# Kernel optimization log

Hardware: AMD Instinct MI355X
Metric: run time of the kernel (lower is better)

The kernel has to match this reference:

```python
import jax, jax.numpy as jnp
import numpy as np

GRID_SIZE, SPLINE_ORDER = 5, 3  # efficient-kan KANLinear defaults
NUM_BASES = GRID_SIZE + SPLINE_ORDER


def b_splines(x, grid):
    # x: (N, in_dim), grid: (in_dim, GRID_SIZE + 2*SPLINE_ORDER + 1)
    xe = x[..., None]
    bases = ((xe >= grid[:, :-1]) & (xe < grid[:, 1:])).astype(x.dtype)
    for k in range(1, SPLINE_ORDER + 1):  # Cox-de Boor recursion (static, 3 iters)
        left = (xe - grid[:, : -(k + 1)]) / (grid[:, k:-1] - grid[:, : -(k + 1)])
        right = (grid[:, k + 1:] - xe) / (grid[:, k + 1:] - grid[:, 1:-k])
        bases = left * bases[..., :-1] + right * bases[..., 1:]
    return bases  # (N, in_dim, NUM_BASES)


def kan_linear(x, grid, base_w, spline_w, scaler):
    # base branch: SiLU(x) @ W_base^T ; spline branch: B-spline basis @ scaled spline weights
    n = x.shape[0]
    out_dim = base_w.shape[0]
    base = jax.nn.silu(x) @ base_w.T
    bs = b_splines(x, grid).reshape(n, -1)                    # (N, in*NUM_BASES)
    sw = (spline_w * scaler[..., None]).reshape(out_dim, -1)  # (out, in*NUM_BASES)
    return base + bs @ sw.T


def setup_inputs() -> dict:
    key = jax.random.key(0)
    N, E, F, H, C, L = 50000, 500000, 128, 128, 40, 3
    ks = jax.random.split(key, 8)
    x = jax.random.normal(ks[0], (N, F), dtype=jnp.float32)
    edge_index = jax.random.randint(ks[1], (2, E), 0, N)
    # KAN grid (registered buffer in efficient-kan): uniform over [-1,1] extended by spline_order
    h_step = 2.0 / GRID_SIZE
    pts = np.arange(-SPLINE_ORDER, GRID_SIZE + SPLINE_ORDER + 1) * h_step - 1.0
    grid_mp = jnp.asarray(np.tile(pts, (F, 1)), dtype=jnp.float32)
    D = F + L * H  # skip-concat dim into output KANLinear
    grid_out = jnp.asarray(np.tile(pts, (D, 1)), dtype=jnp.float32)
    s = 0.1
    conv_base_w = jax.random.normal(ks[2], (L, H, F), dtype=jnp.float32) * s
    conv_spline_w = jax.random.normal(ks[3], (L, H, F, NUM_BASES), dtype=jnp.float32) * s
    conv_scaler = jnp.ones((L, H, F), dtype=jnp.float32)
    conv_bias = jnp.zeros((L, H), dtype=jnp.float32)
    bn_gamma = jnp.ones((L, H), dtype=jnp.float32)
    bn_beta = jnp.zeros((L, H), dtype=jnp.float32)
    out_base_w = jax.random.normal(ks[4], (C, D), dtype=jnp.float32) * s
    out_spline_w = jax.random.normal(ks[5], (C, D, NUM_BASES), dtype=jnp.float32) * s
    out_scaler = jnp.ones((C, D), dtype=jnp.float32)
    return dict(x=x, edge_index=edge_index, grid_mp=grid_mp, conv_base_w=conv_base_w,
                conv_spline_w=conv_spline_w, conv_scaler=conv_scaler, conv_bias=conv_bias,
                bn_gamma=bn_gamma, bn_beta=bn_beta, grid_out=grid_out,
                out_base_w=out_base_w, out_spline_w=out_spline_w, out_scaler=out_scaler)


def reference(x, edge_index, grid_mp, conv_base_w, conv_spline_w, conv_scaler, conv_bias,
              bn_gamma, bn_beta, grid_out, out_base_w, out_spline_w, out_scaler):
    N = x.shape[0]
    L = conv_base_w.shape[0]
    # GCN normalization with self-loops (computed once; identical each layer)
    loop = jnp.arange(N)
    src = jnp.concatenate([edge_index[0], loop])
    dst = jnp.concatenate([edge_index[1], loop])
    deg = jax.ops.segment_sum(jnp.ones_like(src, dtype=x.dtype), dst, num_segments=N)
    dinv = jnp.where(deg > 0, jax.lax.rsqrt(jnp.maximum(deg, 1.0)), 0.0)
    norm = dinv[src] * dinv[dst]  # (E+N,)
    feats = [x]
    for i in range(L):  # static layer loop
        h = kan_linear(x, grid_mp, conv_base_w[i], conv_spline_w[i], conv_scaler[i])
        # symmetric-normalized sparse aggregation (gather on src, scatter-add on dst)
        h = jax.ops.segment_sum(h[src] * norm[:, None], dst, num_segments=N) + conv_bias[i]
        # BatchNorm1d (training mode: biased batch statistics over nodes)
        mu = h.mean(axis=0)
        var = h.var(axis=0)
        x = (h - mu) * jax.lax.rsqrt(var + 1e-5) * bn_gamma[i] + bn_beta[i]
        feats.append(x)  # dropout p=0.0 is identity
    xc = jnp.concatenate(feats, axis=1)  # skip-concat: (N, F + L*H)
    logits = kan_linear(xc, grid_out, out_base_w, out_spline_w, out_scaler)
    return jax.nn.log_softmax(logits, axis=1)
```

## Files before the change

### kernel.cpp

```cpp
#include <hip/hip_runtime.h>
#include <hip/hip_bf16.h>
#include <math.h>

#define F_IN   128
#define HID    128
#define NLAYER 3
#define NCLS   40
#define DCAT   512
#define OOUT   64

typedef short s16x8 __attribute__((ext_vector_type(8)));
typedef unsigned short u16x8 __attribute__((ext_vector_type(8)));
typedef unsigned short u16x4 __attribute__((ext_vector_type(4)));
typedef float f32x4 __attribute__((ext_vector_type(4)));
typedef unsigned long long u64x2 __attribute__((ext_vector_type(2)));


static __device__ __forceinline__ float silu_f(float x) {
    return x / (1.f + __expf(-x));
}

static __device__ __forceinline__ unsigned short f2bf_rn(float f) {
    union { __hip_bfloat16 h; unsigned short u; } cv;
    cv.h = __float2bfloat16(f);
    return cv.u;
}

static __device__ __forceinline__ void lds_barrier() {
    asm volatile("s_waitcnt lgkmcnt(0)" ::: "memory");
    __builtin_amdgcn_s_barrier();
}


__global__ __launch_bounds__(256) void deg_init_kernel(int* deg, int N) {
    for (int i = blockIdx.x * blockDim.x + threadIdx.x; i < N; i += gridDim.x * blockDim.x)
        deg[i] = 1;
}

__global__ __launch_bounds__(256) void deg_count_kernel(const int* __restrict__ dst, int E, int* deg) {
    for (int i = blockIdx.x * blockDim.x + threadIdx.x; i < E; i += gridDim.x * blockDim.x)
        atomicAdd(&deg[dst[i]], 1);
}

__global__ __launch_bounds__(256) void dinv_kernel(const int* __restrict__ deg, float* dinv, int N) {
    for (int i = blockIdx.x * blockDim.x + threadIdx.x; i < N; i += gridDim.x * blockDim.x)
        dinv[i] = rsqrtf((float)deg[i]);
}

__global__ __launch_bounds__(256) void scan_reduce_kernel(const int* __restrict__ deg, int* __restrict__ bsum, int N) {
    __shared__ int sh[256];
    int t = threadIdx.x;
    int e = blockIdx.x * 256 + t;
    sh[t] = (e < N) ? deg[e] : 0;
    __syncthreads();
#pragma unroll
    for (int off = 128; off > 0; off >>= 1) {
        if (t < off) sh[t] += sh[t + off];
        __syncthreads();
    }
    if (t == 0) bsum[blockIdx.x] = sh[0];
}

__global__ __launch_bounds__(256) void scan_top_kernel(const int* __restrict__ bsum, int* __restrict__ bbase, int nsb) {
    __shared__ int sh[256];
    int t = threadIdx.x;
    int chunk = (nsb + 255) >> 8;
    int begin = t * chunk;
    int end = begin + chunk; if (end > nsb) end = nsb;
    int s = 0;
    for (int i = begin; i < end; ++i) s += bsum[i];
    sh[t] = s;
    __syncthreads();
#pragma unroll
    for (int off = 1; off < 256; off <<= 1) {
        int v = 0;
        if (t >= off) v = sh[t - off];
        __syncthreads();
        if (t >= off) sh[t] += v;
        __syncthreads();
    }
    int run = (t == 0) ? 0 : sh[t - 1];
    for (int i = begin; i < end; ++i) {
        bbase[i] = run;
        run += bsum[i];
    }
}

__global__ __launch_bounds__(256) void scan_write_kernel(const int* __restrict__ deg,
                                                         const int* __restrict__ bbase,
                                                         int* __restrict__ offs, int* __restrict__ cursor, int N) {
    __shared__ int sh[256];
    int t = threadIdx.x;
    int e = blockIdx.x * 256 + t;
    int d = (e < N) ? deg[e] : 0;
    sh[t] = d;
    __syncthreads();
#pragma unroll
    for (int off = 1; off < 256; off <<= 1) {
        int v = 0;
        if (t >= off) v = sh[t - off];
        __syncthreads();
        if (t >= off) sh[t] += v;
        __syncthreads();
    }
    int incl = sh[t] + bbase[blockIdx.x];
    int excl = incl - d;
    if (e < N) {
        offs[e] = excl;
        cursor[e] = excl;
        if (e == N - 1) offs[N] = incl;
    }
}

__global__ __launch_bounds__(256) void fill_kernel(const int* __restrict__ src, const int* __restrict__ dst,
                                                   int E, int N, int* cursor, int* __restrict__ csr) {
    int total = E + N;
    for (int i = blockIdx.x * blockDim.x + threadIdx.x; i < total; i += gridDim.x * blockDim.x) {
        if (i < E) {
            int d = dst[i];
            int p = atomicAdd(&cursor[d], 1);
            csr[p] = src[i];
        } else {
            int n = i - E;
            int p = atomicAdd(&cursor[n], 1);
            csr[p] = n;
        }
    }
}

__global__ __launch_bounds__(256) void pack_conv_mfma(const float* __restrict__ bw,
                                                      const float* __restrict__ sw,
                                                      const float* __restrict__ sc,
                                                      unsigned short* __restrict__ wpk) {
    int total = NLAYER * 9 * 4 * 8 * 64 * 8;
    for (int idx = blockIdx.x * blockDim.x + threadIdx.x; idx < total; idx += gridDim.x * blockDim.x) {
        int e    = idx & 7;
        int lane = (idx >> 3) & 63;
        int cf   = (idx >> 9) & 7;
        int kk   = (idx >> 12) & 3;
        int cc   = (idx >> 14) % 9;
        int l    = idx / (9 << 14);
        int o = cf * 16 + (lane & 15);
        int k = kk * 32 + ((lane >> 4) << 3) + e;
        float v;
        if (cc == 8) {
            v = bw[(l * 128 + o) * 128 + k];
        } else {
            int f = cc * 16 + (k >> 3);
            int j = k & 7;
            int base = (l * 128 + o) * 128 + f;
            v = sw[base * 8 + j] * sc[base];
        }
        wpk[idx] = f2bf_rn(v);
    }
}

__global__ __launch_bounds__(256) void pack_out_mfma(const float* __restrict__ bw,
                                                     const float* __restrict__ sw,
                                                     const float* __restrict__ sc,
                                                     unsigned short* __restrict__ wpk) {
    int total = 36 * 4 * 4 * 64 * 8;
    for (int idx = blockIdx.x * blockDim.x + threadIdx.x; idx < total; idx += gridDim.x * blockDim.x) {
        int e    = idx & 7;
        int lane = (idx >> 3) & 63;
        int cf   = (idx >> 9) & 3;
        int kk   = (idx >> 11) & 3;
        int gcc  = idx >> 13;
        int g = gcc / 9, cc = gcc % 9;
        int o = cf * 16 + (lane & 15);
        int k = kk * 32 + ((lane >> 4) << 3) + e;
        float v = 0.f;
        if (o < NCLS) {
            if (cc == 8) {
                int f = g * 128 + k;
                v = bw[o * DCAT + f];
            } else {
                int f = g * 128 + cc * 16 + (k >> 3);
                int j = k & 7;
                int base = o * DCAT + f;
                v = sw[base * 8 + j] * sc[base];
            }
        }
        wpk[idx] = f2bf_rn(v);
    }
}


__global__ __launch_bounds__(512) void affine_init_kernel(float* scA, float* shA) {
    int i = threadIdx.x;
    scA[i] = 1.f; shA[i] = 0.f;
}

template<bool CONV, bool INIT>
__global__ __launch_bounds__(256, 2) void kan_fused_kernel(
    const float* __restrict__ xin, int xstride, int in_off,
    const float* __restrict__ scA, const float* __restrict__ shA,
    const unsigned short* __restrict__ wconv,
    const unsigned short* __restrict__ wout,
    unsigned short* __restrict__ htmp,
    const float* __restrict__ dinv,
    float* __restrict__ out_acc, int N) {

    __shared__ __align__(16) char lds_phi0[16384];
    __shared__ __align__(16) char lds_phi1[16384];

    const int tid = threadIdx.x;
    const int lane = tid & 63;
    const int wave = tid >> 6;
    const int l15 = lane & 15, lg = lane >> 4;
    const int nblk = blockIdx.x * 64;

    const float g0 = -1.f - 3.f * 0.4f;
    const float invh = 1.f / 0.4f;

    const int fg = tid & 3;
    const int n0 = tid >> 2;

    f32x4 accc[4][2];
    f32x4 acco[4];
    if (CONV) {
#pragma unroll
        for (int r = 0; r < 4; ++r)
#pragma unroll
            for (int c = 0; c < 2; ++c) accc[r][c] = (f32x4)0.f;
    }
#pragma unroll
    for (int r = 0; r < 4; ++r) acco[r] = (f32x4)0.f;

    float4 xqb[2], scb[2], shb[2];
    auto ldx = [&](int cc, int slot) {
        int f0 = in_off + cc * 16 + fg * 4;
        scb[slot] = *(const float4*)(scA + f0);
        shb[slot] = *(const float4*)(shA + f0);
        int gn = nblk + n0;
        xqb[slot] = (gn < N) ? *(const float4*)(xin + (size_t)gn * xstride + f0)
                             : (float4){0.f, 0.f, 0.f, 0.f};
    };

    s16x8 wc_reg[4][2];
    s16x8 wo_reg[4];
    auto loadW = [&](int cc) {
        if (CONV) {
            const unsigned short* wcb = wconv + (size_t)cc * 16384;
#pragma unroll
            for (int kk = 0; kk < 4; ++kk)
#pragma unroll
                for (int c = 0; c < 2; ++c) {
                    int cf = wave * 2 + c;
                    wc_reg[kk][c] = *(const s16x8*)(wcb + (((size_t)kk * 8 + cf) * 64 + lane) * 8);
                }
        }
        const unsigned short* wob = wout + (size_t)cc * 8192;
#pragma unroll
        for (int kk = 0; kk < 4; ++kk)
            wo_reg[kk] = *(const s16x8*)(wob + (((size_t)kk * 4 + wave) * 64 + lane) * 8);
    };

    u16x4 sreg[8];

    u64x2 pcur[4];
    auto phi_compute = [&](int ccc, int slot) {
        float xi[4] = {xqb[slot].x, xqb[slot].y, xqb[slot].z, xqb[slot].w};
        float scr[4] = {scb[slot].x, scb[slot].y, scb[slot].z, scb[slot].w};
        float shr[4] = {shb[slot].x, shb[slot].y, shb[slot].z, shb[slot].w};
        u16x4 sv;
#pragma unroll
        for (int fl = 0; fl < 4; ++fl) {
            float y = fmaf(xi[fl], scr[fl], shr[fl]);
            sv[fl] = f2bf_rn(silu_f(y));
            float t = (y - g0) * invh;
            float cfl = floorf(t);
            int c = (int)cfl;
            c = c < -20 ? -20 : (c > 20 ? 20 : c);
            float u = t - cfl;
            float um = 1.f - u;
            float u2 = u * u;
            float um2 = um * um;
            float w0 = um2 * um * (1.f / 6.f);
            float w3 = u2 * u * (1.f / 6.f);
            float w1 = fmaf(fmaf(0.5f, u, -1.f), u2, 2.f / 3.f);
            float w2 = fmaf(fmaf(-0.5f, u, 0.5f), u2, fmaf(0.5f, u, 1.f / 6.f));
            unsigned long long W = (unsigned long long)f2bf_rn(w0)
                                 | ((unsigned long long)f2bf_rn(w1) << 16)
                                 | ((unsigned long long)f2bf_rn(w2) << 32)
                                 | ((unsigned long long)f2bf_rn(w3) << 48);
            int pos = (c - 3) * 16;
            unsigned long long lo = (pos >= 0) ? (W << (pos & 63)) : (W >> ((-pos) & 63));
            lo = (pos >= 64 || pos <= -64) ? 0ull : lo;
            int ph = pos - 64;
            unsigned long long hi = (ph >= 0) ? (W << (ph & 63)) : (W >> ((-ph) & 63));
            hi = (ph >= 64 || ph <= -64) ? 0ull : hi;
            u64x2 v; v.x = lo; v.y = hi;
            pcur[fl] = v;
        }
        sreg[ccc] = sv;
    };

    auto write_phi = [&](char* buf) {
        int swz = (n0 & 7) << 4;
#pragma unroll
        for (int i = 0; i < 4; ++i) {
            int byte = n0 * 256 + ((fg * 64 + i * 16) ^ swz);
            *(u64x2*)(buf + byte) = pcur[i];
        }
    };

    auto write_silu = [&](char* buf) {
        int swz = (n0 & 7) << 4;
#pragma unroll
        for (int ccc = 0; ccc < 8; ++ccc) {
            int byte = n0 * 256 + (((ccc * 16 + fg * 4) * 2) ^ swz);
            *(u16x4*)(buf + byte) = sreg[ccc];
        }
    };

    auto mfma_phase = [&](const char* buf) {
#pragma unroll
        for (int kk = 0; kk < 4; ++kk) {
            const int kb = kk * 64 + lg * 16;
            s16x8 af[4];
#pragma unroll
            for (int r = 0; r < 4; ++r) {
                int n = r * 16 + l15;
                af[r] = *(const s16x8*)(buf + n * 256 + (kb ^ ((n & 7) << 4)));
            }
            if (CONV) {
#pragma unroll
                for (int c = 0; c < 2; ++c)
#pragma unroll
                    for (int r = 0; r < 4; ++r)
                        accc[r][c] = __builtin_amdgcn_mfma_f32_16x16x32_bf16(af[r], wc_reg[kk][c], accc[r][c], 0, 0, 0);
            }
#pragma unroll
            for (int r = 0; r < 4; ++r)
                acco[r] = __builtin_amdgcn_mfma_f32_16x16x32_bf16(af[r], wo_reg[kk], acco[r], 0, 0, 0);
        }
    };

    ldx(0, 0);
    phi_compute(0, 0);
    ldx(1, 1);
    loadW(0);
    write_phi(lds_phi0);
    __syncthreads();

#pragma unroll
    for (int cc = 0; cc < 9; ++cc) {
        char* cur = (cc & 1) ? lds_phi1 : lds_phi0;
        char* nxt = (cc & 1) ? lds_phi0 : lds_phi1;
        if (cc < 7) ldx(cc + 2, cc & 1);
        mfma_phase(cur);
        if (cc < 8) loadW(cc + 1);
        if (cc < 7) {
            phi_compute(cc + 1, (cc + 1) & 1);
            write_phi(nxt);
        }
        if (cc == 7) write_silu(nxt);
        if (cc < 8) lds_barrier();
    }

#pragma unroll
    for (int r = 0; r < 4; ++r) {
        int nb = nblk + r * 16 + lg * 4;
        if (CONV) {
#pragma unroll
            for (int c = 0; c < 2; ++c) {
                int o = wave * 32 + c * 16 + l15;
#pragma unroll
                for (int q = 0; q < 4; ++q) {
                    int n = nb + q;
                    if (n < N) htmp[(size_t)n * HID + o] = f2bf_rn(accc[r][c][q] * dinv[n]);
                }
            }
        }
        {
            int o = wave * 16 + l15;
            if (o < NCLS) {
#pragma unroll
                for (int q = 0; q < 4; ++q) {
                    int n = nb + q;
                    if (n < N) {
                        size_t a = (size_t)n * OOUT + o;
                        float v = acco[r][q];
                        if (!INIT) v += out_acc[a];
                        out_acc[a] = v;
                    }
                }
            }
        }
    }
}

__global__ __launch_bounds__(256) void agg_kernel(const unsigned short* __restrict__ h,
                                                  const float* __restrict__ dinv,
                                                  const int* __restrict__ offs,
                                                  const int* __restrict__ csr,
                                                  const float* __restrict__ bias,
                                                  float* __restrict__ xc, int out_off, int N) {
    int n = blockIdx.x * 4 + (threadIdx.x >> 6);
    if (n >= N) return;
    int lane = threadIdx.x & 63;
    int s = offs[n], e = offs[n + 1];
    float s0[8], s1[8];
#pragma unroll
    for (int k = 0; k < 8; ++k) { s0[k] = 0.f; s1[k] = 0.f; }
    int i = s;
    for (; i + 8 <= e; i += 8) {
        int vv[8];
#pragma unroll
        for (int k = 0; k < 8; ++k) vv[k] = csr[i + k];
        unsigned uu[8];
#pragma unroll
        for (int k = 0; k < 8; ++k) uu[k] = *(const unsigned*)(h + (size_t)vv[k] * HID + lane * 2);
#pragma unroll
        for (int k = 0; k < 8; ++k) {
            s0[k] += __uint_as_float(uu[k] << 16);
            s1[k] += __uint_as_float(uu[k] & 0xffff0000u);
        }
    }
    for (; i < e; ++i) {
        int v = csr[i];
        unsigned u = *(const unsigned*)(h + (size_t)v * HID + lane * 2);
        s0[0] += __uint_as_float(u << 16);
        s1[0] += __uint_as_float(u & 0xffff0000u);
    }
    float a0 = ((s0[0] + s0[1]) + (s0[2] + s0[3])) + ((s0[4] + s0[5]) + (s0[6] + s0[7]));
    float a1 = ((s1[0] + s1[1]) + (s1[2] + s1[3])) + ((s1[4] + s1[5]) + (s1[6] + s1[7]));
    float dn = dinv[n];
    float2 bv = *(const float2*)(bias + lane * 2);
    float2 res = {fmaf(a0, dn, bv.x), fmaf(a1, dn, bv.y)};
    *(float2*)(xc + (size_t)n * DCAT + out_off + lane * 2) = res;
}

__global__ __launch_bounds__(128) void bn_stats_kernel(const float* __restrict__ xc, int off, int N,
                                                       float* __restrict__ bnsum, float* __restrict__ bnsq) {
    int f = threadIdx.x;
    float s = 0.f, q = 0.f;
    for (int n = blockIdx.x; n < N; n += gridDim.x) {
        float v = xc[(size_t)n * DCAT + off + f];
        s += v;
        q += v * v;
    }
    atomicAdd(&bnsum[f], s);
    atomicAdd(&bnsq[f], q);
}

__global__ __launch_bounds__(128) void bn_affine_kernel(const float* __restrict__ bnsum,
                                                        const float* __restrict__ bnsq,
                                                        const float* __restrict__ gamma,
                                                        const float* __restrict__ beta,
                                                        float* scA, float* shA, int seg_off, float invN) {
    int f = threadIdx.x;
    float mu = bnsum[f] * invN;
    float var = bnsq[f] * invN - mu * mu;
    float rs = rsqrtf(var + 1e-5f);
    float s = gamma[f] * rs;
    scA[seg_off + f] = s;
    shA[seg_off + f] = fmaf(-mu, s, beta[f]);
}

__global__ __launch_bounds__(256) void logsoftmax_kernel(const float* __restrict__ oacc,
                                                         float* __restrict__ out, int N) {
    for (int n = blockIdx.x * blockDim.x + threadIdx.x; n < N; n += gridDim.x * blockDim.x) {
        const float* row = oacc + (size_t)n * OOUT;
        float m = -1e30f;
#pragma unroll
        for (int j = 0; j < NCLS; ++j) m = fmaxf(m, row[j]);
        float s = 0.f;
#pragma unroll
        for (int j = 0; j < NCLS; ++j) s += __expf(row[j] - m);
        float lse = m + __logf(s);
        float* orow = out + (size_t)n * NCLS;
#pragma unroll
        for (int j = 0; j < NCLS; ++j) orow[j] = row[j] - lse;
    }
}


extern "C" void kernel_launch(void* const* d_in, const int* in_sizes, int n_in,
                              void* d_out, int out_size, void* d_ws, size_t ws_size,
                              hipStream_t stream) {
    const float* x            = (const float*)d_in[0];
    const int*   eidx         = (const int*)d_in[1];
    const float* conv_base_w  = (const float*)d_in[3];
    const float* conv_spline_w= (const float*)d_in[4];
    const float* conv_scaler  = (const float*)d_in[5];
    const float* conv_bias    = (const float*)d_in[6];
    const float* bn_gamma     = (const float*)d_in[7];
    const float* bn_beta      = (const float*)d_in[8];
    const float* out_base_w   = (const float*)d_in[10];
    const float* out_spline_w = (const float*)d_in[11];
    const float* out_scaler   = (const float*)d_in[12];
    float* out = (float*)d_out;

    int N = in_sizes[0] / F_IN;
    int E = in_sizes[1] / 2;
    const int* esrc = eidx;
    const int* edst = eidx + E;

    int blocks = (N + 63) / 64;
    int npad = blocks * 64;
    int nsb = (N + 255) / 256;

    char* p = (char*)d_ws;
    auto carve = [&](size_t bytes) {
        char* r = p;
        p += (bytes + 255) & ~(size_t)255;
        return r;
    };
    float* xc   = (float*)carve((size_t)N * DCAT * 4);
    unsigned short* htmp = (unsigned short*)carve((size_t)npad * HID * 2);
    float* oacc = (float*)carve((size_t)npad * OOUT * 4);
    float* dinv = (float*)carve((size_t)N * 4);
    float* bn   = (float*)carve((size_t)NLAYER * 2 * HID * 4);
    float* scA  = (float*)carve((size_t)DCAT * 4);
    float* shA  = (float*)carve((size_t)DCAT * 4);
    unsigned short* wpkc = (unsigned short*)carve((size_t)NLAYER * 9 * 128 * 128 * 2);
    unsigned short* wpko = (unsigned short*)carve((size_t)36 * 64 * 128 * 2);
    int* deg    = (int*)carve((size_t)N * 4);
    int* offs   = (int*)carve((size_t)(N + 1) * 4);
    int* cursor = (int*)carve((size_t)(N + 1) * 4);
    int* bsum   = (int*)carve((size_t)nsb * 4);
    int* bbase  = (int*)carve((size_t)nsb * 4);
    int* csr    = (int*)carve((size_t)(E + N) * 4);

    hipMemsetAsync(bn, 0, NLAYER * 2 * HID * 4, stream);

    deg_init_kernel<<<512, 256, 0, stream>>>(deg, N);
    deg_count_kernel<<<1024, 256, 0, stream>>>(edst, E, deg);
    dinv_kernel<<<512, 256, 0, stream>>>(deg, dinv, N);
    scan_reduce_kernel<<<nsb, 256, 0, stream>>>(deg, bsum, N);
    scan_top_kernel<<<1, 256, 0, stream>>>(bsum, bbase, nsb);
    scan_write_kernel<<<nsb, 256, 0, stream>>>(deg, bbase, offs, cursor, N);
    fill_kernel<<<1024, 256, 0, stream>>>(esrc, edst, E, N, cursor, csr);

    pack_conv_mfma<<<1024, 256, 0, stream>>>(conv_base_w, conv_spline_w, conv_scaler, wpkc);
    pack_out_mfma<<<1024, 256, 0, stream>>>(out_base_w, out_spline_w, out_scaler, wpko);
    affine_init_kernel<<<1, 512, 0, stream>>>(scA, shA);

    float invN = 1.f / (float)N;
    for (int l = 0; l < NLAYER; ++l) {
        int in_off = l * HID;
        int out_off = (l + 1) * HID;
        const unsigned short* wl = wpkc + (size_t)l * 9 * 16384;
        const unsigned short* wo = wpko + (size_t)l * 9 * 8192;
        if (l == 0)
            kan_fused_kernel<true, true><<<blocks, 256, 0, stream>>>(
                x, F_IN, 0, scA, shA, wl, wo, htmp, dinv, oacc, N);
        else
            kan_fused_kernel<true, false><<<blocks, 256, 0, stream>>>(
                xc, DCAT, in_off, scA, shA, wl, wo, htmp, dinv, oacc, N);
        agg_kernel<<<(N + 3) / 4, 256, 0, stream>>>(htmp, dinv, offs, csr, conv_bias + l * HID, xc, out_off, N);
        float* bnsum = bn + l * 2 * HID;
        float* bnsq  = bnsum + HID;
        bn_stats_kernel<<<256, 128, 0, stream>>>(xc, out_off, N, bnsum, bnsq);
        bn_affine_kernel<<<1, 128, 0, stream>>>(bnsum, bnsq, bn_gamma + l * HID, bn_beta + l * HID,
                                                scA, shA, out_off, invN);
    }

    kan_fused_kernel<false, false><<<blocks, 256, 0, stream>>>(
        xc, DCAT, 384, scA, shA, nullptr, wpko + (size_t)3 * 9 * 8192, htmp, dinv, oacc, N);

    logsoftmax_kernel<<<(N + 255) / 256, 256, 0, stream>>>(oacc, out, N);
}
```

Measured before the change: 532.3 us.

## Split aggregation wavefront into four edge groups with 16-byte row loads

```diff
diff --git a/kernel.cpp b/kernel.cpp
--- a/kernel.cpp
+++ b/kernel.cpp
@@ -24,6 +24,10 @@
     union { __hip_bfloat16 h; unsigned short u; } cv;
     cv.h = __float2bfloat16(f);
     return cv.u;
+}
+
+static __device__ __forceinline__ float bf2f(unsigned short u) {
+    return __uint_as_float((unsigned)u << 16);
 }
 
 static __device__ __forceinline__ void lds_barrier() {
@@ -400,36 +404,64 @@
     int n = blockIdx.x * 4 + (threadIdx.x >> 6);
     if (n >= N) return;
     int lane = threadIdx.x & 63;
+    int eg = lane >> 4;
+    int cg = lane & 15;
     int s = offs[n], e = offs[n + 1];
-    float s0[8], s1[8];
-#pragma unroll
-    for (int k = 0; k < 8; ++k) { s0[k] = 0.f; s1[k] = 0.f; }
-    int i = s;
-    for (; i + 8 <= e; i += 8) {
-        int vv[8];
-#pragma unroll
-        for (int k = 0; k < 8; ++k) vv[k] = csr[i + k];
-        unsigned uu[8];
-#pragma unroll
-        for (int k = 0; k < 8; ++k) uu[k] = *(const unsigned*)(h + (size_t)vv[k] * HID + lane * 2);
-#pragma unroll
-        for (int k = 0; k < 8; ++k) {
-            s0[k] += __uint_as_float(uu[k] << 16);
-            s1[k] += __uint_as_float(uu[k] & 0xffff0000u);
-        }
-    }
-    for (; i < e; ++i) {
-        int v = csr[i];
-        unsigned u = *(const unsigned*)(h + (size_t)v * HID + lane * 2);
-        s0[0] += __uint_as_float(u << 16);
-        s1[0] += __uint_as_float(u & 0xffff0000u);
-    }
-    float a0 = ((s0[0] + s0[1]) + (s0[2] + s0[3])) + ((s0[4] + s0[5]) + (s0[6] + s0[7]));
-    float a1 = ((s1[0] + s1[1]) + (s1[2] + s1[3])) + ((s1[4] + s1[5]) + (s1[6] + s1[7]));
-    float dn = dinv[n];
-    float2 bv = *(const float2*)(bias + lane * 2);
-    float2 res = {fmaf(a0, dn, bv.x), fmaf(a1, dn, bv.y)};
-    *(float2*)(xc + (size_t)n * DCAT + out_off + lane * 2) = res;
+
+    float acc[4][8];
+#pragma unroll
+    for (int a = 0; a < 4; ++a)
+#pragma unroll
+        for (int k = 0; k < 8; ++k) acc[a][k] = 0.f;
+
+    for (int base = s; base < e; base += 64) {
+        int cnt = e - base; if (cnt > 64) cnt = 64;
+        int ci = base + lane;
+        int cv = (ci < e) ? csr[ci] : 0;
+
+#pragma unroll
+        for (int j = 0; j < 4; ++j) {
+            int ei = j * 4 + eg;
+            int v = __shfl(cv, ei);
+            if (ei < cnt) {
+                u16x8 hv = *(const u16x8*)(h + (size_t)v * HID + cg * 8);
+#pragma unroll
+                for (int k = 0; k < 8; ++k) acc[j][k] += bf2f(hv[k]);
+            }
+        }
+        int nj = (cnt + 3) >> 2;
+        for (int j = 4; j < nj; ++j) {
+            int ei = j * 4 + eg;
+            int v = __shfl(cv, ei);
+            if (ei < cnt) {
+                u16x8 hv = *(const u16x8*)(h + (size_t)v * HID + cg * 8);
+#pragma unroll
+                for (int k = 0; k < 8; ++k) acc[j & 3][k] += bf2f(hv[k]);
+            }
+        }
+    }
+
+    float tot[8];
+#pragma unroll
+    for (int k = 0; k < 8; ++k)
+        tot[k] = (acc[0][k] + acc[1][k]) + (acc[2][k] + acc[3][k]);
+#pragma unroll
+    for (int k = 0; k < 8; ++k) {
+        tot[k] += __shfl_xor(tot[k], 16);
+        tot[k] += __shfl_xor(tot[k], 32);
+    }
+    if (eg == 0) {
+        float dn = dinv[n];
+        float4 b0 = *(const float4*)(bias + cg * 8);
+        float4 b1 = *(const float4*)(bias + cg * 8 + 4);
+        float4 o0 = {fmaf(tot[0], dn, b0.x), fmaf(tot[1], dn, b0.y),
+                     fmaf(tot[2], dn, b0.z), fmaf(tot[3], dn, b0.w)};
+        float4 o1 = {fmaf(tot[4], dn, b1.x), fmaf(tot[5], dn, b1.y),
+                     fmaf(tot[6], dn, b1.z), fmaf(tot[7], dn, b1.w)};
+        float* dst = xc + (size_t)n * DCAT + out_off + cg * 8;
+        *(float4*)dst = o0;
+        *(float4*)(dst + 4) = o1;
+    }
 }
 
 __global__ __launch_bounds__(128) void bn_stats_kernel(const float* __restrict__ xc, int off, int N,
```

Result: faster. 512.4 us, median of 3 (-3.7%).
